# Kernel tuning notes

Hardware: AMD Instinct MI355X
Metric: run time of the kernel (lower is better)

## Reference

```python
import jax, jax.numpy as jnp
import numpy as np

E = 256          # embedding_dim
IN = E + 1       # input feature dim (embedding_dim + 1)
B = 128          # batch
N = 1027         # nodes: 1 source + 1024 candidates + 1 destination + 1 depot
REWIRE_P = 0.1


def setup_inputs() -> dict:
    key = jax.random.key(0)
    ks = jax.random.split(key, 16)
    scale = 1.0 / np.sqrt(IN)

    def lin_w(k):
        return jax.random.normal(k, (E, IN), dtype=jnp.float32) * scale

    def lin_b(k):
        return jax.random.normal(k, (E,), dtype=jnp.float32) * scale

    # sparse small-world rewiring weights: nc scalar writes -> one scatter
    nc = int(IN * E * REWIRE_P)  # 6579
    rows = jax.random.randint(ks[10], (nc,), 0, E)
    cols = jax.random.randint(ks[11], (nc,), 0, IN)
    vals = jax.random.normal(ks[12], (nc,), dtype=jnp.float32) * 0.01
    W_rand = jnp.zeros((E, IN), dtype=jnp.float32).at[rows, cols].set(vals)

    return {
        "solutions": jax.random.normal(ks[0], (B, N, IN), dtype=jnp.float32),
        "W_src": lin_w(ks[1]), "b_src": lin_b(ks[2]),
        "W_dst": lin_w(ks[3]), "b_dst": lin_b(ks[4]),
        "W_dep": lin_w(ks[5]), "b_dep": lin_b(ks[6]),
        "W_cand": lin_w(ks[7]), "b_cand": lin_b(ks[8]),
        "W_reg": lin_w(ks[9]), "b_reg": lin_b(ks[13]),
        "W_rand": W_rand,
        "integration_weight": jnp.float32(0.3),
    }


def reference(solutions, W_src, b_src, W_dst, b_dst, W_dep, b_dep,
              W_cand, b_cand, W_reg, b_reg, W_rand, integration_weight):
    # slice node groups: [B,1,IN], [B,N-3,IN], [B,1,IN], [B,1,IN]
    src = solutions[:, :1, :]
    cand = solutions[:, 1:-2, :]
    dst = solutions[:, -2:-1, :]
    dep = solutions[:, -1:, :]

    def lin(x, W, b):
        return jnp.einsum('bnd,ed->bne', x, W) + b

    def sw(x):
        # SmallWorldLayer: regular linear + 0.1 * sparse random matmul
        return lin(x, W_reg, b_reg) + 0.1 * jnp.einsum('bnd,ed->bne', x, W_rand)

    alpha = jax.nn.sigmoid(integration_weight)

    def mix(emb, sw_out):
        return (1.0 - alpha) * emb + alpha * sw_out

    source_emb = mix(lin(src, W_src, b_src), sw(src))
    candidates_emb = mix(lin(cand, W_cand, b_cand), sw(cand))
    destination_emb = mix(lin(dst, W_dst, b_dst), sw(dst))
    depot_emb = mix(lin(dep, W_dep, b_dep), sw(dep))
    return (source_emb, candidates_emb, destination_emb, depot_emb)
```

## Files before the change

kernel.cpp:

```cpp
#include <hip/hip_runtime.h>
#include <hip/hip_bf16.h>

typedef __bf16 bf16x8 __attribute__((ext_vector_type(8)));
typedef __bf16 bf16x4 __attribute__((ext_vector_type(4)));
typedef float  f32x4  __attribute__((ext_vector_type(4)));
typedef float  f32x4u __attribute__((ext_vector_type(4), aligned(4)));

#define BATCH 128
#define NSOL  1027
#define IND   257
#define EMB   256
#define OUT_SRC  0ULL
#define OUT_CAND 32768ULL
#define OUT_DST  33587200ULL
#define OUT_DEP  33619968ULL

#define WFRAG_OFF 0
#define BEFF_OFF  131072
#define WT_OFF    135168

#define XSTRIDE_B 528
#define X256_OFF  16896
#define SMEM_BYTES 17024

__global__ __launch_bounds__(256) void swne_prep(
    const float* __restrict__ Wsrc, const float* __restrict__ bsrc,
    const float* __restrict__ Wdst, const float* __restrict__ bdst,
    const float* __restrict__ Wdep, const float* __restrict__ bdep,
    const float* __restrict__ Wcand, const float* __restrict__ bcand,
    const float* __restrict__ Wreg, const float* __restrict__ breg,
    const float* __restrict__ Wrand, const float* __restrict__ iw,
    char* __restrict__ ws)
{
    const float a  = 1.0f / (1.0f + expf(-iw[0]));
    const float ca = 1.0f - a;
    const float sa = 0.1f * a;

    const float* Ws[4] = {Wsrc, Wcand, Wdst, Wdep};
    const float* Bs[4] = {bsrc, bcand, bdst, bdep};

    const int gid = blockIdx.x * 256 + threadIdx.x;
    const int gsz = gridDim.x * 256;

    float* beff = (float*)(ws + BEFF_OFF);
    for (int i = gid; i < 4 * EMB; i += gsz) {
        int seg = i >> 8, e = i & 255;
        beff[i] = ca * Bs[seg][e] + a * breg[e];
    }

    float* wt = (float*)(ws + WT_OFF);
    for (int i = gid; i < 4 * IND * EMB; i += gsz) {
        int seg = i / (IND * EMB);
        int rem = i - seg * (IND * EMB);
        int k = rem >> 8, e = rem & 255;
        int si = e * IND + k;
        wt[i] = ca * Ws[seg][si] + a * Wreg[si] + sa * Wrand[si];
    }

    __bf16* wfr = (__bf16*)(ws + WFRAG_OFF);
    for (int i = gid; i < 8 * 16 * 64 * 8; i += gsz) {
        int kk   = i >> 13;
        int rem  = i & 8191;
        int ntg  = rem >> 9;
        int rem2 = rem & 511;
        int l    = rem2 >> 3;
        int j    = rem2 & 7;
        int e = ntg * 16 + (l & 15);
        int k = kk * 32 + (l >> 4) * 8 + j;
        int si = e * IND + k;
        wfr[i] = (__bf16)(ca * Wcand[si] + a * Wreg[si] + sa * Wrand[si]);
    }
}

__global__ __launch_bounds__(256, 4) void swne_main(const float* __restrict__ sol,
                                                    const char* __restrict__ ws,
                                                    float* __restrict__ out)
{
    __shared__ __align__(16) char smem[SMEM_BYTES];
    const int tid = threadIdx.x;
    const int bid = blockIdx.x;
    const float* beff = (const float*)(ws + BEFF_OFF);

    if (bid < 384) {
        float* xrow = (float*)smem;
        int s = bid >> 7;
        int b = bid & 127;
        int nrow  = (s == 0) ? 0 : (s == 1 ? 1025 : 1026);
        int segw  = (s == 0) ? 0 : (s == 1 ? 2 : 3);
        size_t outb = (s == 0) ? OUT_SRC : (s == 1 ? OUT_DST : OUT_DEP);
        const float* x = sol + (size_t)(b * NSOL + nrow) * IND;
        for (int i = tid; i < IND; i += 256) xrow[i] = x[i];
        __syncthreads();
        const float* wtp = (const float*)(ws + WT_OFF) + (size_t)segw * (IND * EMB) + tid;
        float s0 = 0.f, s1 = 0.f, s2 = 0.f, s3 = 0.f;
        #pragma unroll 4
        for (int k = 0; k < 256; k += 4) {
            s0 = fmaf(xrow[k + 0], wtp[(size_t)(k + 0) * 256], s0);
            s1 = fmaf(xrow[k + 1], wtp[(size_t)(k + 1) * 256], s1);
            s2 = fmaf(xrow[k + 2], wtp[(size_t)(k + 2) * 256], s2);
            s3 = fmaf(xrow[k + 3], wtp[(size_t)(k + 3) * 256], s3);
        }
        float sum = beff[segw * 256 + tid] + ((s0 + s1) + (s2 + s3))
                  + xrow[256] * wtp[(size_t)256 * 256];
        out[outb + (size_t)b * 256 + tid] = sum;
        return;
    }

    const int cb = bid - 384;
    const int bb = cb >> 5;
    const int t  = cb & 31;
    const int lane = tid & 63, wave = tid >> 6;
    const int rl = lane & 15, grp = lane >> 4;

    const float* tbase = sol + ((size_t)bb * NSOL + 1 + t * 32) * IND;

    #pragma unroll
    for (int rr = 0; rr < 8; ++rr) {
        const int r = wave * 8 + rr;
        f32x4u v = *((const f32x4u*)(tbase + (size_t)r * IND) + lane);
        bf16x4 h;
        h[0] = (__bf16)v[0]; h[1] = (__bf16)v[1];
        h[2] = (__bf16)v[2]; h[3] = (__bf16)v[3];
        *(bf16x4*)(smem + r * XSTRIDE_B + lane * 8) = h;
    }
    if (tid < 32)
        *(float*)(smem + X256_OFF + tid * 4) = tbase[(size_t)tid * IND + 256];
    __syncthreads();

    f32x4 acc[2][4];
    #pragma unroll
    for (int rt = 0; rt < 2; ++rt)
        #pragma unroll
        for (int n = 0; n < 4; ++n) {
            f32x4 z = {0.f, 0.f, 0.f, 0.f};
            acc[rt][n] = z;
        }

    const bf16x8* wf8 = (const bf16x8*)(ws + WFRAG_OFF);

    #pragma unroll
    for (int kk = 0; kk < 8; ++kk) {
        bf16x8 a0 = *(const bf16x8*)(smem + rl * XSTRIDE_B + kk * 64 + grp * 16);
        bf16x8 a1 = *(const bf16x8*)(smem + (16 + rl) * XSTRIDE_B + kk * 64 + grp * 16);
        #pragma unroll
        for (int n = 0; n < 4; ++n) {
            bf16x8 wv = wf8[(size_t)((kk * 16 + wave * 4 + n) * 64 + lane)];
            acc[0][n] = __builtin_amdgcn_mfma_f32_16x16x32_bf16(wv, a0, acc[0][n], 0, 0, 0);
            acc[1][n] = __builtin_amdgcn_mfma_f32_16x16x32_bf16(wv, a1, acc[1][n], 0, 0, 0);
        }
    }

    const float* bc   = beff + 256;
    const float* w256 = (const float*)(ws + WT_OFF) + (size_t)(IND * EMB) + 256 * 256;
    const int ecol = wave * 64 + grp * 4;

    #pragma unroll
    for (int rt = 0; rt < 2; ++rt) {
        const int row = rt * 16 + rl;
        const float xl = *(const float*)(smem + X256_OFF + row * 4);
        float* op = out + OUT_CAND + ((size_t)bb * 1024 + t * 32 + row) * 256 + ecol;
        #pragma unroll
        for (int n = 0; n < 4; ++n) {
            f32x4 b4 = *(const f32x4*)(bc + ecol + n * 16);
            f32x4 w4 = *(const f32x4*)(w256 + ecol + n * 16);
            f32x4 r = acc[rt][n] + xl * w4 + b4;
            *(f32x4*)(op + n * 16) = r;
        }
    }
}

extern "C" void kernel_launch(void* const* d_in, const int* in_sizes, int n_in,
                              void* d_out, int out_size, void* d_ws, size_t ws_size,
                              hipStream_t stream) {
    const float* sol   = (const float*)d_in[0];
    const float* Wsrc  = (const float*)d_in[1];
    const float* bsrc  = (const float*)d_in[2];
    const float* Wdst  = (const float*)d_in[3];
    const float* bdst  = (const float*)d_in[4];
    const float* Wdep  = (const float*)d_in[5];
    const float* bdep  = (const float*)d_in[6];
    const float* Wcand = (const float*)d_in[7];
    const float* bcand = (const float*)d_in[8];
    const float* Wreg  = (const float*)d_in[9];
    const float* breg  = (const float*)d_in[10];
    const float* Wrand = (const float*)d_in[11];
    const float* iw    = (const float*)d_in[12];

    swne_prep<<<512, 256, 0, stream>>>(Wsrc, bsrc, Wdst, bdst, Wdep, bdep,
                                       Wcand, bcand, Wreg, breg, Wrand, iw,
                                       (char*)d_ws);
    swne_main<<<4480, 256, 0, stream>>>(sol, (const char*)d_ws, (float*)d_out);
}
```

Measured before the change: 73.57 us.

## Persistent 512-thread blocks with register-resident weights and double-buffered input tiles

The main kernel now uses 512-thread blocks that each process four 32-row candidate tiles. Each block holds its bf16 weight fragments in registers and prefetches the next tile into a second shared-memory buffer while the current tile runs through MFMA. The source, destination and depot rows go through the same MFMA path in batches of 32 rather than through a scalar fp32 dot-product path, and the prep kernel no longer builds the full transposed fp32 weight matrix. The aim is to cut repeated weight loads and the launch of many small blocks, and to hide input load latency. In exchange it raises register pressure and computes the three single-row groups in bf16, which lowers their precision.

```diff
diff --git a/kernel.cpp b/kernel.cpp
--- a/kernel.cpp
+++ b/kernel.cpp
@@ -16,12 +16,13 @@
 #define OUT_DEP  33619968ULL
 
 #define WFRAG_OFF 0
-#define BEFF_OFF  131072
-#define WT_OFF    135168
-
-#define XSTRIDE_B 528
-#define X256_OFF  16896
-#define SMEM_BYTES 17024
+#define WFRAG_SEG 131072
+#define BEFF_OFF  524288
+#define W256_OFF  528384
+
+#define XST_B     528
+#define X256_OFF_B 16896
+#define BUF_B     17024
 
 __global__ __launch_bounds__(256) void swne_prep(
     const float* __restrict__ Wsrc, const float* __restrict__ bsrc,
@@ -43,129 +44,139 @@
     const int gsz = gridDim.x * 256;
 
     float* beff = (float*)(ws + BEFF_OFF);
+    float* w256 = (float*)(ws + W256_OFF);
     for (int i = gid; i < 4 * EMB; i += gsz) {
         int seg = i >> 8, e = i & 255;
         beff[i] = ca * Bs[seg][e] + a * breg[e];
-    }
-
-    float* wt = (float*)(ws + WT_OFF);
-    for (int i = gid; i < 4 * IND * EMB; i += gsz) {
-        int seg = i / (IND * EMB);
-        int rem = i - seg * (IND * EMB);
-        int k = rem >> 8, e = rem & 255;
-        int si = e * IND + k;
-        wt[i] = ca * Ws[seg][si] + a * Wreg[si] + sa * Wrand[si];
+        int si = e * IND + 256;
+        w256[i] = ca * Ws[seg][si] + a * Wreg[si] + sa * Wrand[si];
     }
 
     __bf16* wfr = (__bf16*)(ws + WFRAG_OFF);
-    for (int i = gid; i < 8 * 16 * 64 * 8; i += gsz) {
-        int kk   = i >> 13;
-        int rem  = i & 8191;
-        int ntg  = rem >> 9;
-        int rem2 = rem & 511;
-        int l    = rem2 >> 3;
-        int j    = rem2 & 7;
-        int e = ntg * 16 + (l & 15);
+    for (int i = gid; i < 4 * 65536; i += gsz) {
+        int seg  = i >> 16;
+        int rem  = i & 65535;
+        int kk   = rem >> 13;
+        int rem2 = rem & 8191;
+        int cg   = rem2 >> 9;
+        int rem3 = rem2 & 511;
+        int l    = rem3 >> 3;
+        int j    = rem3 & 7;
+        int e = cg * 16 + (l & 15);
         int k = kk * 32 + (l >> 4) * 8 + j;
         int si = e * IND + k;
-        wfr[i] = (__bf16)(ca * Wcand[si] + a * Wreg[si] + sa * Wrand[si]);
+        wfr[i] = (__bf16)(ca * Ws[seg][si] + a * Wreg[si] + sa * Wrand[si]);
     }
 }
 
-__global__ __launch_bounds__(256, 4) void swne_main(const float* __restrict__ sol,
+#define BARRIER() { asm volatile("s_waitcnt lgkmcnt(0)" ::: "memory"); \
+  __builtin_amdgcn_s_barrier(); asm volatile("" ::: "memory"); }
+
+#define ISSUE(xb, pf, pf256) { \
+  _Pragma("unroll") for (int rr = 0; rr < 4; ++rr) \
+    pf[rr] = *((const f32x4u*)((xb) + (size_t)(wave * 4 + rr) * xstr) + lane); \
+  if (tid < 32) pf256 = (xb)[(size_t)tid * xstr + 256]; }
+
+#define WRITEB(b, pf, pf256) { \
+  _Pragma("unroll") for (int rr = 0; rr < 4; ++rr) { \
+    const int r_ = wave * 4 + rr; \
+    bf16x4 h_; \
+    h_[0] = (__bf16)pf[rr][0]; h_[1] = (__bf16)pf[rr][1]; \
+    h_[2] = (__bf16)pf[rr][2]; h_[3] = (__bf16)pf[rr][3]; \
+    *(bf16x4*)(smem + (b) * BUF_B + r_ * XST_B + lane * 8) = h_; } \
+  if (tid < 32) *(float*)(smem + (b) * BUF_B + X256_OFF_B + tid * 4) = pf256; }
+
+__global__ __launch_bounds__(512, 4) void swne_main(const float* __restrict__ sol,
                                                     const char* __restrict__ ws,
                                                     float* __restrict__ out)
 {
-    __shared__ __align__(16) char smem[SMEM_BYTES];
-    const int tid = threadIdx.x;
-    const int bid = blockIdx.x;
-    const float* beff = (const float*)(ws + BEFF_OFF);
-
-    if (bid < 384) {
-        float* xrow = (float*)smem;
-        int s = bid >> 7;
-        int b = bid & 127;
-        int nrow  = (s == 0) ? 0 : (s == 1 ? 1025 : 1026);
-        int segw  = (s == 0) ? 0 : (s == 1 ? 2 : 3);
-        size_t outb = (s == 0) ? OUT_SRC : (s == 1 ? OUT_DST : OUT_DEP);
-        const float* x = sol + (size_t)(b * NSOL + nrow) * IND;
-        for (int i = tid; i < IND; i += 256) xrow[i] = x[i];
-        __syncthreads();
-        const float* wtp = (const float*)(ws + WT_OFF) + (size_t)segw * (IND * EMB) + tid;
-        float s0 = 0.f, s1 = 0.f, s2 = 0.f, s3 = 0.f;
-        #pragma unroll 4
-        for (int k = 0; k < 256; k += 4) {
-            s0 = fmaf(xrow[k + 0], wtp[(size_t)(k + 0) * 256], s0);
-            s1 = fmaf(xrow[k + 1], wtp[(size_t)(k + 1) * 256], s1);
-            s2 = fmaf(xrow[k + 2], wtp[(size_t)(k + 2) * 256], s2);
-            s3 = fmaf(xrow[k + 3], wtp[(size_t)(k + 3) * 256], s3);
-        }
-        float sum = beff[segw * 256 + tid] + ((s0 + s1) + (s2 + s3))
-                  + xrow[256] * wtp[(size_t)256 * 256];
-        out[outb + (size_t)b * 256 + tid] = sum;
-        return;
-    }
-
-    const int cb = bid - 384;
-    const int bb = cb >> 5;
-    const int t  = cb & 31;
+    __shared__ __align__(16) char smem[2 * BUF_B];
+    const int tid = threadIdx.x, bid = blockIdx.x;
     const int lane = tid & 63, wave = tid >> 6;
     const int rl = lane & 15, grp = lane >> 4;
 
-    const float* tbase = sol + ((size_t)bb * NSOL + 1 + t * 32) * IND;
-
+    const float* xbase; size_t xstr; float* obase; int seg, ntiles;
+    size_t tstep_x, tstep_o;
+    if (bid < 12) {
+        const int s3 = bid >> 2;
+        seg = (s3 == 0) ? 0 : (s3 == 1 ? 2 : 3);
+        const int nrow = (s3 == 0) ? 0 : (s3 == 1 ? 1025 : 1026);
+        const size_t outb = (s3 == 0) ? OUT_SRC : (s3 == 1 ? OUT_DST : OUT_DEP);
+        const int b0 = (bid & 3) * 32;
+        xbase = sol + ((size_t)b0 * NSOL + nrow) * IND;
+        xstr  = (size_t)NSOL * IND;
+        obase = out + outb + (size_t)b0 * 256;
+        ntiles = 1; tstep_x = 0; tstep_o = 0;
+    } else {
+        const int c = bid - 12;
+        seg = 1;
+        const int t0 = c * 4;
+        const int bb = t0 >> 5, tr0 = t0 & 31;
+        xbase = sol + ((size_t)bb * NSOL + 1 + tr0 * 32) * IND;
+        xstr  = IND;
+        obase = out + OUT_CAND + ((size_t)bb * 1024 + tr0 * 32) * 256;
+        ntiles = 4;
+        tstep_x = (size_t)32 * IND;
+        tstep_o = (size_t)32 * 256;
+    }
+
+    const bf16x8* wfs = (const bf16x8*)(ws + WFRAG_OFF) + (size_t)seg * 8192;
+    bf16x8 wreg[8][2];
     #pragma unroll
-    for (int rr = 0; rr < 8; ++rr) {
-        const int r = wave * 8 + rr;
-        f32x4u v = *((const f32x4u*)(tbase + (size_t)r * IND) + lane);
-        bf16x4 h;
-        h[0] = (__bf16)v[0]; h[1] = (__bf16)v[1];
-        h[2] = (__bf16)v[2]; h[3] = (__bf16)v[3];
-        *(bf16x4*)(smem + r * XSTRIDE_B + lane * 8) = h;
-    }
-    if (tid < 32)
-        *(float*)(smem + X256_OFF + tid * 4) = tbase[(size_t)tid * IND + 256];
-    __syncthreads();
-
-    f32x4 acc[2][4];
-    #pragma unroll
-    for (int rt = 0; rt < 2; ++rt)
-        #pragma unroll
-        for (int n = 0; n < 4; ++n) {
-            f32x4 z = {0.f, 0.f, 0.f, 0.f};
-            acc[rt][n] = z;
+    for (int kk = 0; kk < 8; ++kk)
+        #pragma unroll
+        for (int n = 0; n < 2; ++n)
+            wreg[kk][n] = wfs[(size_t)((kk * 16 + wave * 2 + n) * 64 + lane)];
+
+    const float* bc = (const float*)(ws + BEFF_OFF) + seg * 256;
+    const float* wc = (const float*)(ws + W256_OFF) + seg * 256;
+
+    f32x4 pfA[4]; float pfA256 = 0.f;
+
+    ISSUE(xbase, pfA, pfA256);
+    WRITEB(0, pfA, pfA256);
+    BARRIER();
+
+    for (int i = 0; i < ntiles; ++i) {
+        const int cb = i & 1;
+        const bool more = (i + 1 < ntiles);
+        if (more) { const float* xn = xbase + (size_t)(i + 1) * tstep_x; ISSUE(xn, pfA, pfA256); }
+
+        f32x4 acc[2][2];
+        #pragma unroll
+        for (int rt = 0; rt < 2; ++rt)
+            #pragma unroll
+            for (int n = 0; n < 2; ++n) {
+                f32x4 z = {0.f, 0.f, 0.f, 0.f};
+                acc[rt][n] = z;
+            }
+        const char* xb = smem + cb * BUF_B;
+        #pragma unroll
+        for (int kk = 0; kk < 8; ++kk) {
+            bf16x8 a0 = *(const bf16x8*)(xb + rl * XST_B + kk * 64 + grp * 16);
+            bf16x8 a1 = *(const bf16x8*)(xb + (16 + rl) * XST_B + kk * 64 + grp * 16);
+            #pragma unroll
+            for (int n = 0; n < 2; ++n) {
+                acc[0][n] = __builtin_amdgcn_mfma_f32_16x16x32_bf16(wreg[kk][n], a0, acc[0][n], 0, 0, 0);
+                acc[1][n] = __builtin_amdgcn_mfma_f32_16x16x32_bf16(wreg[kk][n], a1, acc[1][n], 0, 0, 0);
+            }
         }
-
-    const bf16x8* wf8 = (const bf16x8*)(ws + WFRAG_OFF);
-
-    #pragma unroll
-    for (int kk = 0; kk < 8; ++kk) {
-        bf16x8 a0 = *(const bf16x8*)(smem + rl * XSTRIDE_B + kk * 64 + grp * 16);
-        bf16x8 a1 = *(const bf16x8*)(smem + (16 + rl) * XSTRIDE_B + kk * 64 + grp * 16);
-        #pragma unroll
-        for (int n = 0; n < 4; ++n) {
-            bf16x8 wv = wf8[(size_t)((kk * 16 + wave * 4 + n) * 64 + lane)];
-            acc[0][n] = __builtin_amdgcn_mfma_f32_16x16x32_bf16(wv, a0, acc[0][n], 0, 0, 0);
-            acc[1][n] = __builtin_amdgcn_mfma_f32_16x16x32_bf16(wv, a1, acc[1][n], 0, 0, 0);
+        float* ob = obase + (size_t)i * tstep_o;
+        #pragma unroll
+        for (int rt = 0; rt < 2; ++rt) {
+            const float xl = *(const float*)(xb + X256_OFF_B + (rt * 16 + rl) * 4);
+            float* op = ob + (size_t)(rt * 16 + rl) * 256 + wave * 32 + grp * 4;
+            #pragma unroll
+            for (int n = 0; n < 2; ++n) {
+                const int e0 = wave * 32 + n * 16 + grp * 4;
+                f32x4 b4 = *(const f32x4*)(bc + e0);
+                f32x4 w4 = *(const f32x4*)(wc + e0);
+                f32x4 r = acc[rt][n] + xl * w4 + b4;
+                *(f32x4*)(op + n * 16) = r;
+            }
         }
-    }
-
-    const float* bc   = beff + 256;
-    const float* w256 = (const float*)(ws + WT_OFF) + (size_t)(IND * EMB) + 256 * 256;
-    const int ecol = wave * 64 + grp * 4;
-
-    #pragma unroll
-    for (int rt = 0; rt < 2; ++rt) {
-        const int row = rt * 16 + rl;
-        const float xl = *(const float*)(smem + X256_OFF + row * 4);
-        float* op = out + OUT_CAND + ((size_t)bb * 1024 + t * 32 + row) * 256 + ecol;
-        #pragma unroll
-        for (int n = 0; n < 4; ++n) {
-            f32x4 b4 = *(const f32x4*)(bc + ecol + n * 16);
-            f32x4 w4 = *(const f32x4*)(w256 + ecol + n * 16);
-            f32x4 r = acc[rt][n] + xl * w4 + b4;
-            *(f32x4*)(op + n * 16) = r;
-        }
+
+        if (more) { WRITEB(cb ^ 1, pfA, pfA256); BARRIER(); }
     }
 }
 
@@ -189,5 +200,5 @@
     swne_prep<<<512, 256, 0, stream>>>(Wsrc, bsrc, Wdst, bdst, Wdep, bdep,
                                        Wcand, bcand, Wreg, breg, Wrand, iw,
                                        (char*)d_ws);
-    swne_main<<<4480, 256, 0, stream>>>(sol, (const char*)d_ws, (float*)d_out);
+    swne_main<<<1036, 512, 0, stream>>>(sol, (const char*)d_ws, (float*)d_out);
 }
```

Measured after the change: 115.1 us. 1.56x slower.
